# Optimization experiments

Measured on AMD Instinct MI355X. Metric: run time of the kernel, lower is better.

## Reference

```python
import jax, jax.numpy as jnp
import numpy as np

M, B, N, C, H = 3, 8, 512, 512, 8
HD = C // H
W_SCALE = 0.02  # keep attention logits in a sane range


def setup_inputs() -> dict:
    key = jax.random.key(0)
    ks = jax.random.split(key, 10)
    f32 = jnp.float32
    return {
        "x": jax.random.normal(ks[0], (M, B, N, C), f32),
        "Wq": jax.random.normal(ks[1], (M, C, C), f32) * W_SCALE,
        "bq": jax.random.normal(ks[2], (M, C), f32) * W_SCALE,
        "Wk": jax.random.normal(ks[3], (M, C, C), f32) * W_SCALE,
        "bk": jax.random.normal(ks[4], (M, C), f32) * W_SCALE,
        "Wv": jax.random.normal(ks[5], (M, C, C), f32) * W_SCALE,
        "bv": jax.random.normal(ks[6], (M, C), f32) * W_SCALE,
        "mw": jnp.ones((M, M), f32),
        "Wp": jax.random.normal(ks[7], (C, C), f32) * W_SCALE,
        "bp": jax.random.normal(ks[8], (C,), f32) * W_SCALE,
    }


def reference(x, Wq, bq, Wk, bk, Wv, bv, mw, Wp, bp):
    # x: [M,B,N,C] stacked modality features
    m, b, n, c = x.shape
    h, hd = H, c // H
    scale = hd ** -0.5

    def project(W, bias):
        y = jnp.einsum('mbnc,mcd->mbnd', x, W) + bias[:, None, None, :]
        return y.reshape(m, b, n, h, hd).transpose(0, 1, 3, 2, 4)  # [M,B,H,N,hd]

    q = project(Wq, bq)
    k = project(Wk, bk)
    v = project(Wv, bv)

    # all M*M pairwise attentions: i = query modality, j = key/value modality
    scores = jnp.einsum('ibhnd,jbhkd->ijbhnk', q, k) * scale  # [M,M,B,H,N,N]
    probs = jax.nn.softmax(scores, axis=-1)
    out = jnp.einsum('ijbhnk,jbhkd->ijbhnd', probs, v)
    out = out * mw[:, :, None, None, None, None]  # per-pair modal weight

    # sum over key-modality j, then mean over query-modality i
    fused = out.sum(axis=1).mean(axis=0)  # [B,H,N,hd]
    fused = fused.transpose(0, 2, 1, 3).reshape(b, n, c)  # [B,N,C]

    return jnp.einsum('bnc,cd->bnd', fused, Wp) + bp
```

## Files before the change

kernel.cpp:

```cpp
#include <hip/hip_runtime.h>
#include <stdint.h>

#define M_ 3
#define B_ 8
#define N_ 512
#define C_ 512
#define H_ 8
#define HD_ 64

typedef __bf16 bf16x8 __attribute__((ext_vector_type(8)));
typedef __bf16 bf16x2 __attribute__((ext_vector_type(2)));
typedef float f32x4 __attribute__((ext_vector_type(4)));
typedef float f32x16 __attribute__((ext_vector_type(16)));
typedef unsigned int u32x4 __attribute__((ext_vector_type(4)));

#if __has_builtin(__builtin_amdgcn_exp2f)
#define EXP2(x) __builtin_amdgcn_exp2f(x)
#else
#define EXP2(x) __expf((x)*0.69314718056f)
#endif

#define K_PRESCALE 0.18033688f

static __device__ __forceinline__ unsigned short f2bf(float f) {
  unsigned int u = __float_as_uint(f);
  unsigned int r = (u + 0x7FFFu + ((u >> 16) & 1u)) >> 16;
  return (unsigned short)r;
}
static __device__ __forceinline__ float bf2f(unsigned short s) {
  return __uint_as_float(((unsigned int)s) << 16);
}

static __device__ __forceinline__ void gll16(const void* g, void* l) {
  __builtin_amdgcn_global_load_lds(
      (const __attribute__((address_space(1))) unsigned int*)g,
      (__attribute__((address_space(3))) unsigned int*)l, 16, 0, 0);
}

__global__ void convert_x_kernel(const float* __restrict__ x,
                                 unsigned short* __restrict__ xb, int n4) {
  int i = blockIdx.x * 256 + threadIdx.x;
  if (i < n4) {
    float4 v = ((const float4*)x)[i];
    ushort4 o;
    o.x = f2bf(v.x); o.y = f2bf(v.y); o.z = f2bf(v.z); o.w = f2bf(v.w);
    ((ushort4*)xb)[i] = o;
  }
}

__global__ void transpose_w_kernel(const float* __restrict__ Wq, const float* __restrict__ Wk,
                                   const float* __restrict__ Wv, const float* __restrict__ Wp,
                                   unsigned short* __restrict__ Wqt, unsigned short* __restrict__ Wkt,
                                   unsigned short* __restrict__ Wvt, unsigned short* __restrict__ Wpt) {
  int z = blockIdx.z;
  const float* src; unsigned short* dst;
  if (z < 3)      { src = Wq + z * 262144;      dst = Wqt + z * 262144; }
  else if (z < 6) { src = Wk + (z - 3) * 262144; dst = Wkt + (z - 3) * 262144; }
  else if (z < 9) { src = Wv + (z - 6) * 262144; dst = Wvt + (z - 6) * 262144; }
  else            { src = Wp;                    dst = Wpt; }
  __shared__ unsigned short t[64][68];
  int r0 = blockIdx.x * 64, c0 = blockIdx.y * 64;
  int tr = threadIdx.x >> 4, tc = (threadIdx.x & 15) * 4;
#pragma unroll
  for (int it = 0; it < 4; ++it) {
    int r = tr + it * 16;
    float4 v = *(const float4*)&src[(size_t)(r0 + r) * 512 + c0 + tc];
    t[tc + 0][r] = f2bf(v.x); t[tc + 1][r] = f2bf(v.y);
    t[tc + 2][r] = f2bf(v.z); t[tc + 3][r] = f2bf(v.w);
  }
  __syncthreads();
#pragma unroll
  for (int it = 0; it < 4; ++it) {
    int d = tr + it * 16;
    ushort4 o;
    o.x = t[d][tc + 0]; o.y = t[d][tc + 1]; o.z = t[d][tc + 2]; o.w = t[d][tc + 3];
    *(ushort4*)&dst[(size_t)(c0 + d) * 512 + r0 + tc] = o;
  }
}

template <int MODE>
__launch_bounds__(256, 2)
__global__ void gemm128_kernel(const unsigned short* __restrict__ Aall,
                               const unsigned short* __restrict__ Bt0,
                               const unsigned short* __restrict__ Bt1,
                               const unsigned short* __restrict__ Bt2,
                               const float* __restrict__ bias0,
                               const float* __restrict__ bias1,
                               const float* __restrict__ bias2,
                               unsigned short* __restrict__ outQ,
                               unsigned short* __restrict__ outK,
                               unsigned short* __restrict__ outVt,
                               float* __restrict__ outF) {
  const int tid = threadIdx.x;
  const int wv = tid >> 6, l = tid & 63;
  const int wr = wv >> 1, wc = wv & 1;
  const int bm = blockIdx.x, bn = blockIdx.y;
  int m = 0, p = 0;
  const unsigned short* A; const unsigned short* Bt; const float* bias;
  if (MODE == 0) {
    int z = blockIdx.z; m = z / 3; p = z % 3;
    A = Aall + (size_t)m * (B_ * N_ * C_);
    Bt = (p == 0 ? Bt0 : p == 1 ? Bt1 : Bt2) + (size_t)m * (C_ * C_);
    bias = (p == 0 ? bias0 : p == 1 ? bias1 : bias2) + m * C_;
  } else {
    A = Aall; Bt = Bt0; bias = bias0;
  }
  __shared__ __align__(16) unsigned short lA[2][128 * 64];
  __shared__ __align__(16) unsigned short lB[2][128 * 64];
  f32x4 acc[4][4] = {};

  auto stage = [&](int buf, int kt) {
    int k0 = kt * 64;
#pragma unroll
    for (int it = 0; it < 4; ++it) {
      int f = (it * 256 + tid) * 16;
      int r = f >> 7, o = f & 127;
      int so = o ^ ((r & 7) << 4);
      gll16((const char*)A + ((size_t)(bm * 128 + r) * 512 + k0) * 2 + so,
            (char*)&lA[buf][0] + (it * 256 + wv * 64) * 16);
      gll16((const char*)Bt + ((size_t)(bn * 128 + r) * 512 + k0) * 2 + so,
            (char*)&lB[buf][0] + (it * 256 + wv * 64) * 16);
    }
  };

  stage(0, 0);
  __syncthreads();
  int buf = 0;
  for (int kt = 0; kt < 8; ++kt) {
    if (kt < 7) stage(buf ^ 1, kt + 1);
    bf16x8 aF[4][2], bF[4][2];
#pragma unroll
    for (int rt = 0; rt < 4; ++rt)
#pragma unroll
      for (int kf = 0; kf < 2; ++kf) {
        int rowA = wr * 64 + rt * 16 + (l & 15);
        int rowB = wc * 64 + rt * 16 + (l & 15);
        int kb = kf * 64 + (l >> 4) * 16;
        aF[rt][kf] = *(const bf16x8*)((const char*)&lA[buf][0] + rowA * 128 + (kb ^ ((rowA & 7) << 4)));
        bF[rt][kf] = *(const bf16x8*)((const char*)&lB[buf][0] + rowB * 128 + (kb ^ ((rowB & 7) << 4)));
      }
#pragma unroll
    for (int kf = 0; kf < 2; ++kf)
#pragma unroll
      for (int rt = 0; rt < 4; ++rt)
#pragma unroll
        for (int ct = 0; ct < 4; ++ct)
          acc[rt][ct] = __builtin_amdgcn_mfma_f32_16x16x32_bf16(aF[rt][kf], bF[ct][kf], acc[rt][ct], 0, 0, 0);
    __syncthreads();
    buf ^= 1;
  }

  const float vscale = (MODE == 0 && p == 1) ? K_PRESCALE : 1.0f;
#pragma unroll
  for (int rt = 0; rt < 4; ++rt) {
    int rbase = bm * 128 + wr * 64 + rt * 16 + (l >> 4) * 4;
#pragma unroll
    for (int ct = 0; ct < 4; ++ct) {
      int col = bn * 128 + wc * 64 + ct * 16 + (l & 15);
      float bb = bias[col];
      if (MODE == 0) {
        int h = col >> 6, hd = col & 63;
        if (p < 2) {
          unsigned short* out = (p == 0 ? outQ : outK) + (size_t)m * (B_ * H_ * N_ * HD_);
#pragma unroll
          for (int jr = 0; jr < 4; ++jr) {
            int row = rbase + jr; int b = row >> 9, n = row & 511;
            out[(((size_t)(b * H_ + h) * N_ + n) * HD_) + hd] = f2bf((acc[rt][ct][jr] + bb) * vscale);
          }
        } else {
          unsigned short* out = outVt + (size_t)m * (B_ * H_ * HD_ * N_);
          int row = rbase; int b = row >> 9, n = row & 511;
          ushort4 o;
          o.x = f2bf(acc[rt][ct][0] + bb);
          o.y = f2bf(acc[rt][ct][1] + bb);
          o.z = f2bf(acc[rt][ct][2] + bb);
          o.w = f2bf(acc[rt][ct][3] + bb);
          *(ushort4*)&out[(((size_t)(b * H_ + h) * HD_ + hd) * N_) + n] = o;
        }
      } else {
#pragma unroll
        for (int jr = 0; jr < 4; ++jr) {
          int row = rbase + jr;
          outF[(size_t)row * C_ + col] = acc[rt][ct][jr] + bb;
        }
      }
    }
  }
}

__launch_bounds__(256, 4)
__global__ void attn_kernel(const unsigned short* __restrict__ qg,
                            const unsigned short* __restrict__ kg,
                            const unsigned short* __restrict__ vg,
                            const float* __restrict__ mw,
                            unsigned short* __restrict__ att9) {
  const int tid = threadIdx.x;
  const int wv = tid >> 6, l = tid & 63;
  const int hi = l >> 5, lq = l & 31;
  const int xcd = blockIdx.x & 7, slot = blockIdx.x >> 3;
  const int bh = (xcd << 3) | (slot & 7);
  const int r_ = slot >> 3;
  const int qt = r_ & 3, ij = r_ >> 2;
  const int i = ij / 3, j = ij % 3;
  const int b = bh >> 3, h = bh & 7;
  const int n0 = qt * 128;

  __shared__ __align__(16) unsigned short lK[2][64 * 64];
  __shared__ __align__(16) unsigned short lV[2][64 * 64];

  bf16x8 qB[4];
  {
    const unsigned short* qb = qg + (size_t)((i * B_ + b) * H_ + h) * N_ * HD_;
    int n = n0 + wv * 32 + lq;
#pragma unroll
    for (int ks = 0; ks < 4; ++ks)
      qB[ks] = *(const bf16x8*)&qb[(size_t)n * HD_ + ks * 16 + hi * 8];
  }
  bf16x8 onesB;
#pragma unroll
  for (int zz = 0; zz < 8; ++zz) onesB[zz] = (__bf16)1.0f;

  const char* kb = (const char*)(kg + (size_t)((j * B_ + b) * H_ + h) * N_ * HD_);
  const char* vb = (const char*)(vg + (size_t)((j * B_ + b) * H_ + h) * HD_ * N_);
  auto stage = [&](int buf, int kt) {
#pragma unroll
    for (int it = 0; it < 2; ++it) {
      int c = it * 256 + tid;
      int fi = c >> 6, ll = c & 63;
      int lo = ll & 31, hh = ll >> 5;
      int kkt2 = fi >> 2, kks = fi & 3;
      gll16(kb + (size_t)(kt * 64 + kkt2 * 32 + lo) * 128 + kks * 32 + hh * 16,
            (char*)&lK[buf][0] + (it * 256 + wv * 64) * 16);
      int vks = fi >> 1, vht = fi & 1;
      gll16(vb + (size_t)(vht * 32 + lo) * 1024 + kt * 128 + vks * 32 + hh * 16,
            (char*)&lV[buf][0] + (it * 256 + wv * 64) * 16);
    }
  };
  stage(0, 0);
  __syncthreads();

  f32x16 oacc[2] = {};
  f32x16 dacc = {};
  int buf = 0;
  for (int kt = 0; kt < 8; ++kt) {
    if (kt < 7) stage(buf ^ 1, kt + 1);
#pragma unroll
    for (int kt2 = 0; kt2 < 2; ++kt2) {
      f32x16 sT = {};
      __builtin_amdgcn_s_setprio(1);
#pragma unroll
      for (int ks = 0; ks < 4; ++ks) {
        bf16x8 kA = *(const bf16x8*)((const char*)&lK[buf][0] + ((kt2 * 4 + ks) * 64 + l) * 16);
        sT = __builtin_amdgcn_mfma_f32_32x32x16_bf16(kA, qB[ks], sT, 0, 0, 0);
      }
      __builtin_amdgcn_s_setprio(0);
      unsigned int c[8];
#pragma unroll
      for (int w = 0; w < 8; ++w) {
        bf16x2 t2;
        t2[0] = (__bf16)EXP2(sT[2 * w]);
        t2[1] = (__bf16)EXP2(sT[2 * w + 1]);
        c[w] = __builtin_bit_cast(unsigned int, t2);
      }
      __builtin_amdgcn_s_setprio(1);
#pragma unroll
      for (int hs = 0; hs < 2; ++hs) {
        int ksg = kt2 * 2 + hs;
        unsigned int s0 = hi ? c[4 * hs + 0] : c[4 * hs + 2];
        unsigned int s1 = hi ? c[4 * hs + 1] : c[4 * hs + 3];
        unsigned int r0 = (unsigned int)__shfl_xor((int)s0, 32, 64);
        unsigned int r1 = (unsigned int)__shfl_xor((int)s1, 32, 64);
        u32x4 pw;
        pw.x = hi ? r0 : c[4 * hs + 0];
        pw.y = hi ? r1 : c[4 * hs + 1];
        pw.z = hi ? c[4 * hs + 2] : r0;
        pw.w = hi ? c[4 * hs + 3] : r1;
        bf16x8 pA = __builtin_bit_cast(bf16x8, pw);
        dacc = __builtin_amdgcn_mfma_f32_32x32x16_bf16(pA, onesB, dacc, 0, 0, 0);
#pragma unroll
        for (int ht = 0; ht < 2; ++ht) {
          bf16x8 vB = *(const bf16x8*)((const char*)&lV[buf][0] + ((ksg * 2 + ht) * 64 + l) * 16);
          oacc[ht] = __builtin_amdgcn_mfma_f32_32x32x16_bf16(pA, vB, oacc[ht], 0, 0, 0);
        }
      }
      __builtin_amdgcn_s_setprio(0);
    }
    __syncthreads();
    buf ^= 1;
  }

  float w = mw[ij] * (1.0f / 3.0f);
  unsigned short* outp = att9 + (size_t)ij * (B_ * N_ * C_);
#pragma unroll
  for (int reg = 0; reg < 16; ++reg) {
    float t = w / dacc[reg];
    int n = n0 + wv * 32 + (reg & 3) + 8 * (reg >> 2) + 4 * hi;
#pragma unroll
    for (int ht = 0; ht < 2; ++ht) {
      int cc = h * 64 + ht * 32 + lq;
      outp[((size_t)b * N_ + n) * C_ + cc] = f2bf(oacc[ht][reg] * t);
    }
  }
}

__global__ void sum9_kernel(const unsigned short* __restrict__ att9,
                            unsigned short* __restrict__ o, int n8) {
  int idx = blockIdx.x * 256 + threadIdx.x;
  if (idx >= n8) return;
  float acc[8] = {};
#pragma unroll
  for (int s = 0; s < 9; ++s) {
    uint4 v = ((const uint4*)(att9 + (size_t)s * (B_ * N_ * C_)))[idx];
    acc[0] += bf2f((unsigned short)(v.x & 0xffff));
    acc[1] += bf2f((unsigned short)(v.x >> 16));
    acc[2] += bf2f((unsigned short)(v.y & 0xffff));
    acc[3] += bf2f((unsigned short)(v.y >> 16));
    acc[4] += bf2f((unsigned short)(v.z & 0xffff));
    acc[5] += bf2f((unsigned short)(v.z >> 16));
    acc[6] += bf2f((unsigned short)(v.w & 0xffff));
    acc[7] += bf2f((unsigned short)(v.w >> 16));
  }
  uint4 r;
  r.x = (unsigned int)f2bf(acc[0]) | ((unsigned int)f2bf(acc[1]) << 16);
  r.y = (unsigned int)f2bf(acc[2]) | ((unsigned int)f2bf(acc[3]) << 16);
  r.z = (unsigned int)f2bf(acc[4]) | ((unsigned int)f2bf(acc[5]) << 16);
  r.w = (unsigned int)f2bf(acc[6]) | ((unsigned int)f2bf(acc[7]) << 16);
  ((uint4*)o)[idx] = r;
}

extern "C" void kernel_launch(void* const* d_in, const int* in_sizes, int n_in,
                              void* d_out, int out_size, void* d_ws, size_t ws_size,
                              hipStream_t stream) {
  const float* x  = (const float*)d_in[0];
  const float* Wq = (const float*)d_in[1];
  const float* bq = (const float*)d_in[2];
  const float* Wk = (const float*)d_in[3];
  const float* bk = (const float*)d_in[4];
  const float* Wv = (const float*)d_in[5];
  const float* bv = (const float*)d_in[6];
  const float* mw = (const float*)d_in[7];
  const float* Wp = (const float*)d_in[8];
  const float* bp = (const float*)d_in[9];
  float* out = (float*)d_out;

  char* ws = (char*)d_ws;
  size_t off = 0;
  auto alloc = [&](size_t elems) {
    unsigned short* pp = (unsigned short*)(ws + off);
    off += elems * 2; off = (off + 255) & ~(size_t)255;
    return pp;
  };
  unsigned short* xb   = alloc((size_t)M_ * B_ * N_ * C_);
  unsigned short* Wqt  = alloc((size_t)M_ * C_ * C_);
  unsigned short* Wkt  = alloc((size_t)M_ * C_ * C_);
  unsigned short* Wvt  = alloc((size_t)M_ * C_ * C_);
  unsigned short* Wpt  = alloc((size_t)C_ * C_);
  unsigned short* qb   = alloc((size_t)M_ * B_ * H_ * N_ * HD_);
  unsigned short* kb   = alloc((size_t)M_ * B_ * H_ * N_ * HD_);
  unsigned short* vtb  = alloc((size_t)M_ * B_ * H_ * HD_ * N_);
  unsigned short* att9 = alloc((size_t)9 * B_ * N_ * C_);
  unsigned short* fb   = alloc((size_t)B_ * N_ * C_);

  convert_x_kernel<<<6144, 256, 0, stream>>>(x, xb, (M_ * B_ * N_ * C_) / 4);
  transpose_w_kernel<<<dim3(8, 8, 10), 256, 0, stream>>>(Wq, Wk, Wv, Wp, Wqt, Wkt, Wvt, Wpt);
  gemm128_kernel<0><<<dim3(32, 4, 9), 256, 0, stream>>>(xb, Wqt, Wkt, Wvt, bq, bk, bv,
                                                        qb, kb, vtb, nullptr);
  attn_kernel<<<2304, 256, 0, stream>>>(qb, kb, vtb, mw, att9);
  sum9_kernel<<<1024, 256, 0, stream>>>(att9, fb, (B_ * N_ * C_) / 8);
  gemm128_kernel<1><<<dim3(32, 4, 1), 256, 0, stream>>>(fb, Wpt, nullptr, nullptr, bp, nullptr, nullptr,
                                                        nullptr, nullptr, nullptr, out);
}
```

Baseline: 202.2 us.

## Merge prep kernels and XOR-swizzle attention K/V LDS tiles

The x conversion and weight transpose kernels are merged into one launch, which removes a kernel launch and its gap. In the attention kernel, K and V tiles are now staged into LDS as row-major 32x128 tiles with an XOR swizzle on 16-byte segments, and the fragment reads use the matching swizzled addresses, to cut LDS bank conflicts. The s_setprio hints around the MFMA sections are also removed. The swizzle changes how the global_load_lds staging addresses map to the MFMA fragment reads, so it has to be exactly consistent or results will be wrong.

```diff
diff --git a/kernel.cpp b/kernel.cpp
--- a/kernel.cpp
+++ b/kernel.cpp
@@ -37,29 +37,29 @@
       (__attribute__((address_space(3))) unsigned int*)l, 16, 0, 0);
 }
 
-__global__ void convert_x_kernel(const float* __restrict__ x,
-                                 unsigned short* __restrict__ xb, int n4) {
-  int i = blockIdx.x * 256 + threadIdx.x;
-  if (i < n4) {
+__global__ void prep_kernel(const float* __restrict__ x,
+                            const float* __restrict__ Wq, const float* __restrict__ Wk,
+                            const float* __restrict__ Wv, const float* __restrict__ Wp,
+                            unsigned short* __restrict__ xb,
+                            unsigned short* __restrict__ Wqt, unsigned short* __restrict__ Wkt,
+                            unsigned short* __restrict__ Wvt, unsigned short* __restrict__ Wpt) {
+  __shared__ unsigned short t[64][68];
+  if (blockIdx.x < 6144) {
+    int i = blockIdx.x * 256 + threadIdx.x;
     float4 v = ((const float4*)x)[i];
     ushort4 o;
     o.x = f2bf(v.x); o.y = f2bf(v.y); o.z = f2bf(v.z); o.w = f2bf(v.w);
     ((ushort4*)xb)[i] = o;
-  }
-}
-
-__global__ void transpose_w_kernel(const float* __restrict__ Wq, const float* __restrict__ Wk,
-                                   const float* __restrict__ Wv, const float* __restrict__ Wp,
-                                   unsigned short* __restrict__ Wqt, unsigned short* __restrict__ Wkt,
-                                   unsigned short* __restrict__ Wvt, unsigned short* __restrict__ Wpt) {
-  int z = blockIdx.z;
+    return;
+  }
+  int tz = blockIdx.x - 6144;
+  int z = tz >> 6, rem = tz & 63;
   const float* src; unsigned short* dst;
-  if (z < 3)      { src = Wq + z * 262144;      dst = Wqt + z * 262144; }
+  if (z < 3)      { src = Wq + z * 262144;       dst = Wqt + z * 262144; }
   else if (z < 6) { src = Wk + (z - 3) * 262144; dst = Wkt + (z - 3) * 262144; }
   else if (z < 9) { src = Wv + (z - 6) * 262144; dst = Wvt + (z - 6) * 262144; }
-  else            { src = Wp;                    dst = Wpt; }
-  __shared__ unsigned short t[64][68];
-  int r0 = blockIdx.x * 64, c0 = blockIdx.y * 64;
+  else            { src = Wp;                     dst = Wpt; }
+  int r0 = (rem >> 3) * 64, c0 = (rem & 7) * 64;
   int tr = threadIdx.x >> 4, tc = (threadIdx.x & 15) * 4;
 #pragma unroll
   for (int it = 0; it < 4; ++it) {
@@ -205,8 +205,8 @@
   const int b = bh >> 3, h = bh & 7;
   const int n0 = qt * 128;
 
-  __shared__ __align__(16) unsigned short lK[2][64 * 64];
-  __shared__ __align__(16) unsigned short lV[2][64 * 64];
+  __shared__ __align__(16) unsigned short lK[2][32 * 128];
+  __shared__ __align__(16) unsigned short lV[2][32 * 128];
 
   bf16x8 qB[4];
   {
@@ -226,13 +226,12 @@
 #pragma unroll
     for (int it = 0; it < 2; ++it) {
       int c = it * 256 + tid;
-      int fi = c >> 6, ll = c & 63;
-      int lo = ll & 31, hh = ll >> 5;
-      int kkt2 = fi >> 2, kks = fi & 3;
-      gll16(kb + (size_t)(kt * 64 + kkt2 * 32 + lo) * 128 + kks * 32 + hh * 16,
+      int row = c >> 4, s = c & 15;
+      int s0 = s ^ (row & 15);
+      int hh = s0 >> 3, d16 = s0 & 7;
+      gll16(kb + (size_t)(kt * 64 + hh * 32 + row) * 128 + d16 * 16,
             (char*)&lK[buf][0] + (it * 256 + wv * 64) * 16);
-      int vks = fi >> 1, vht = fi & 1;
-      gll16(vb + (size_t)(vht * 32 + lo) * 1024 + kt * 128 + vks * 32 + hh * 16,
+      gll16(vb + (size_t)(hh * 32 + row) * 1024 + kt * 128 + d16 * 16,
             (char*)&lV[buf][0] + (it * 256 + wv * 64) * 16);
     }
   };
@@ -247,13 +246,12 @@
 #pragma unroll
     for (int kt2 = 0; kt2 < 2; ++kt2) {
       f32x16 sT = {};
-      __builtin_amdgcn_s_setprio(1);
 #pragma unroll
       for (int ks = 0; ks < 4; ++ks) {
-        bf16x8 kA = *(const bf16x8*)((const char*)&lK[buf][0] + ((kt2 * 4 + ks) * 64 + l) * 16);
+        int sK = (kt2 * 8 + ks * 2 + hi) ^ (lq & 15);
+        bf16x8 kA = *(const bf16x8*)((const char*)&lK[buf][0] + lq * 256 + sK * 16);
         sT = __builtin_amdgcn_mfma_f32_32x32x16_bf16(kA, qB[ks], sT, 0, 0, 0);
       }
-      __builtin_amdgcn_s_setprio(0);
       unsigned int c[8];
 #pragma unroll
       for (int w = 0; w < 8; ++w) {
@@ -262,14 +260,13 @@
         t2[1] = (__bf16)EXP2(sT[2 * w + 1]);
         c[w] = __builtin_bit_cast(unsigned int, t2);
       }
-      __builtin_amdgcn_s_setprio(1);
 #pragma unroll
       for (int hs = 0; hs < 2; ++hs) {
         int ksg = kt2 * 2 + hs;
-        unsigned int s0 = hi ? c[4 * hs + 0] : c[4 * hs + 2];
-        unsigned int s1 = hi ? c[4 * hs + 1] : c[4 * hs + 3];
-        unsigned int r0 = (unsigned int)__shfl_xor((int)s0, 32, 64);
-        unsigned int r1 = (unsigned int)__shfl_xor((int)s1, 32, 64);
+        unsigned int s0_ = hi ? c[4 * hs + 0] : c[4 * hs + 2];
+        unsigned int s1_ = hi ? c[4 * hs + 1] : c[4 * hs + 3];
+        unsigned int r0 = (unsigned int)__shfl_xor((int)s0_, 32, 64);
+        unsigned int r1 = (unsigned int)__shfl_xor((int)s1_, 32, 64);
         u32x4 pw;
         pw.x = hi ? r0 : c[4 * hs + 0];
         pw.y = hi ? r1 : c[4 * hs + 1];
@@ -279,11 +276,11 @@
         dacc = __builtin_amdgcn_mfma_f32_32x32x16_bf16(pA, onesB, dacc, 0, 0, 0);
 #pragma unroll
         for (int ht = 0; ht < 2; ++ht) {
-          bf16x8 vB = *(const bf16x8*)((const char*)&lV[buf][0] + ((ksg * 2 + ht) * 64 + l) * 16);
+          int sV = (ht * 8 + ksg * 2 + hi) ^ (lq & 15);
+          bf16x8 vB = *(const bf16x8*)((const char*)&lV[buf][0] + lq * 256 + sV * 16);
           oacc[ht] = __builtin_amdgcn_mfma_f32_32x32x16_bf16(pA, vB, oacc[ht], 0, 0, 0);
         }
       }
-      __builtin_amdgcn_s_setprio(0);
     }
     __syncthreads();
     buf ^= 1;
@@ -361,8 +358,7 @@
   unsigned short* att9 = alloc((size_t)9 * B_ * N_ * C_);
   unsigned short* fb   = alloc((size_t)B_ * N_ * C_);
 
-  convert_x_kernel<<<6144, 256, 0, stream>>>(x, xb, (M_ * B_ * N_ * C_) / 4);
-  transpose_w_kernel<<<dim3(8, 8, 10), 256, 0, stream>>>(Wq, Wk, Wv, Wp, Wqt, Wkt, Wvt, Wpt);
+  prep_kernel<<<6784, 256, 0, stream>>>(x, Wq, Wk, Wv, Wp, xb, Wqt, Wkt, Wvt, Wpt);
   gemm128_kernel<0><<<dim3(32, 4, 9), 256, 0, stream>>>(xb, Wqt, Wkt, Wvt, bq, bk, bv,
                                                         qb, kb, vtb, nullptr);
   attn_kernel<<<2304, 256, 0, stream>>>(qb, kb, vtb, mw, att9);
```

Result: faster. 195.9 us (-3.1%).
